# Kernel tuning notes

Hardware: AMD Instinct MI355X
Metric: run time of the kernel (lower is better)

The kernel has to match this reference:

```python
import jax, jax.numpy as jnp
import numpy as np

NB, H, C = 6, 4, 192
B, S, L = 2, 64, 256
VOCAB, ED = 24, 64


def setup_inputs() -> dict:
    key = jax.random.key(0)
    ks = iter(jax.random.split(key, 32))
    r = lambda sh: jax.random.normal(next(ks), sh, jnp.float32) * 0.02
    z = lambda sh: jnp.zeros(sh, jnp.float32)
    return {
        'tokens': jax.random.randint(next(ks), (B, S, L), 0, VOCAB, jnp.int32),
        'emb': r((VOCAB, ED)),
        'proj_w': r((C, ED)), 'proj_b': z((C,)),
        'ln_g': jnp.ones((NB, 3, C), jnp.float32), 'ln_b': z((NB, 3, C)),
        'wq': r((NB, 2, C, C)), 'wk': r((NB, 2, C, C)),
        'wv': r((NB, 2, C, C)), 'wo': r((NB, 2, C, C)),
        'bq': z((NB, 2, C)), 'bk': z((NB, 2, C)),
        'bv': z((NB, 2, C)), 'bo': z((NB, 2, C)),
        'ffn_w1': r((NB, 4 * C, C)), 'ffn_b1': z((NB, 4 * C)),
        'ffn_w2': r((NB, C, 4 * C)), 'ffn_b2': z((NB, C)),
        'pw_w': r((C,)), 'pw_b': z(()),
    }


def rotary(x):
    # ESM-style rotary embedding over positions along dim -2, feature dim last.
    d = x.shape[-1]
    inv = 1.0 / (10000.0 ** (jnp.arange(0, d, 2, dtype=jnp.float32) / d))
    t = jnp.arange(x.shape[-2], dtype=jnp.float32)
    f = t[:, None] * inv[None, :]                  # (pos, d/2)
    emb = jnp.concatenate([f, f], axis=-1)         # (pos, d)
    cos, sin = jnp.cos(emb), jnp.sin(emb)
    x1, x2 = jnp.split(x, 2, axis=-1)
    return x * cos + jnp.concatenate([-x2, x1], axis=-1) * sin


def ln_ch(x, g, b, eps=1e-5):
    # LayerNorm over channel axis 1 of (B,C,X,Y) (== transpose->LN->transpose).
    m = x.mean(axis=1, keepdims=True)
    v = jnp.var(x, axis=1, keepdims=True)
    return (x - m) * jax.lax.rsqrt(v + eps) * g[None, :, None, None] + b[None, :, None, None]


def lin_attn(x, wq, wk, wv, wo, bq, bk, bv, bo):
    # ScaledLinearAttention: elu+1 feature map, attends over dim -2 of (B,A,N,C).
    Bm, A, N, Cm = x.shape
    dh = Cm // H
    sh = lambda t: t.reshape(Bm, A, N, H, dh).transpose(0, 1, 3, 2, 4)  # (B,A,H,N,dh)
    q = sh(x @ wq.T + bq)
    k = sh(x @ wk.T + bk)
    v = sh(x @ wv.T + bv)
    q = (jax.nn.elu(q) + 1.0) / jnp.sqrt(jnp.float32(dh))
    k = jax.nn.elu(k) + 1.0
    kv = jnp.einsum('bahnd,bahne->bahde', k, v)
    z = 1.0 / (jnp.einsum('bahnd,bahd->bahn', q, k.sum(axis=-2)) + 1e-6)
    o = jnp.einsum('bahnd,bahde->bahne', q, kv) * z[..., None]
    o = o.transpose(0, 1, 3, 2, 4).reshape(Bm, A, N, Cm)
    return o @ wo.T + bo


def fwd(tokens, emb, proj_w, proj_b, ln_g, ln_b, wq, wk, wv, wo, bq, bk, bv, bo,
        ffn_w1, ffn_b1, ffn_w2, ffn_b2, pw_w, pw_b):
    x = emb[tokens]                    # (B,S,L,ED)
    x = x @ proj_w.T + proj_b          # (B,S,L,C)
    x = rotary(x)                      # rotary over L positions
    out = jnp.transpose(x, (0, 3, 1, 2))  # (B,C,S,L)
    for i in range(NB):
        # row attention (over L)
        h = ln_ch(out, ln_g[i, 0], ln_b[i, 0])
        h = jnp.transpose(h, (0, 2, 3, 1))  # (B,S,L,C)
        h = lin_attn(h, wq[i, 0], wk[i, 0], wv[i, 0], wo[i, 0],
                     bq[i, 0], bk[i, 0], bv[i, 0], bo[i, 0])
        out = out + jnp.transpose(h, (0, 3, 1, 2))
        # col attention (over S)
        h = ln_ch(out, ln_g[i, 1], ln_b[i, 1])
        h = jnp.transpose(h, (0, 3, 2, 1))  # (B,L,S,C)
        h = lin_attn(h, wq[i, 1], wk[i, 1], wv[i, 1], wo[i, 1],
                     bq[i, 1], bk[i, 1], bv[i, 1], bo[i, 1])
        out = out + jnp.transpose(h, (0, 3, 2, 1))
        # 1x1-conv FFN
        h = ln_ch(out, ln_g[i, 2], ln_b[i, 2])
        h = jnp.einsum('bcxy,oc->boxy', h, ffn_w1[i]) + ffn_b1[i][None, :, None, None]
        h = jax.nn.gelu(h, approximate=False)
        h = jnp.einsum('bcxy,oc->boxy', h, ffn_w2[i]) + ffn_b2[i][None, :, None, None]
        out = out + h
    o = jnp.einsum('bcxy,c->bxy', out, pw_w) + pw_b   # pwFNN 1x1 conv to 1 ch
    return jax.nn.sigmoid(jax.nn.softplus(o))


def reference(tokens, emb, proj_w, proj_b, ln_g, ln_b, wq, wk, wv, wo, bq, bk, bv, bo,
              ffn_w1, ffn_b1, ffn_w2, ffn_b2, pw_w, pw_b):
    return fwd(tokens, emb, proj_w, proj_b, ln_g, ln_b, wq, wk, wv, wo, bq, bk, bv, bo,
               ffn_w1, ffn_b1, ffn_w2, ffn_b2, pw_w, pw_b)
```

## Files before the change

### kernel.cpp

```cpp
#include <hip/hip_runtime.h>
#include <hip/hip_bf16.h>
#include <math.h>

#define NBLK 6
#define NH 4
#define CCH 192
#define BB 2
#define SS 64
#define LL 256
#define DH 48
#define NP (BB*SS*LL)
#define BUF ((size_t)NP*CCH)

typedef __attribute__((ext_vector_type(8))) short short8;
typedef __attribute__((ext_vector_type(4))) float float4v;

__device__ __forceinline__ unsigned short f2b(float f) {
    union { float f; unsigned int u; } v; v.f = f;
    unsigned int r = v.u + 0x7FFF + ((v.u >> 16) & 1);
    return (unsigned short)(r >> 16);
}
__device__ __forceinline__ float b2f(unsigned short u) {
    union { unsigned int u; float f; } v; v.u = ((unsigned int)u) << 16;
    return v.f;
}
__device__ __forceinline__ void async_lds16(const void* g, void* l) {
    __builtin_amdgcn_global_load_lds(
        (const __attribute__((address_space(1))) unsigned int*)g,
        (__attribute__((address_space(3))) unsigned int*)l, 16, 0, 0);
}

template<int N, int K>
__global__ void swz_conv(const float* __restrict__ src, unsigned short* __restrict__ dst, int layers) {
    int s = blockIdx.x * 256 + threadIdx.x;
    if (s >= layers * N * K) return;
    int li = s / (N * K);
    int t = s - li * (N * K);
    constexpr int KC = K / 32;
    int chunk = t >> 9, c = t & 511;
    int g = chunk / KC, sk = chunk - g * KC;
    int lane = c >> 3, ko = c & 7;
    int n = g * 16 + (lane & 15), k = sk * 32 + (lane >> 4) * 8 + ko;
    dst[s] = f2b(src[(size_t)li * N * K + (size_t)n * K + k]);
}
__global__ void wqkv_swz(const float* __restrict__ wq, const float* __restrict__ wk,
                         const float* __restrict__ wv, unsigned short* __restrict__ d) {
    int s = blockIdx.x * 256 + threadIdx.x;
    int wi = s / (576 * 192);
    int t = s - wi * 576 * 192;
    int chunk = t >> 9, c = t & 511;
    int g = chunk / 6, sk = chunk - g * 6;
    int lane = c >> 3, ko = c & 7;
    int n = g * 16 + (lane & 15), k = sk * 32 + (lane >> 4) * 8 + ko;
// ... 27 lines not shown
    int p = blockIdx.x * 4 + wave;
    int l = p & (LL - 1);
    const float* xp = Xt + (size_t)p * CCH;
    float v[3];
    #pragma unroll
    for (int i = 0; i < 3; ++i) {
        int c = lane + i * 64;
        int j = c % 96;
        float inv = expf((float)(2 * j) * (-9.210340371976184f / 192.0f));
        float ang = (float)l * inv;
        float part = (c < 96) ? -xp[c + 96] : xp[c - 96];
        v[i] = xp[c] * cosf(ang) + part * sinf(ang);
    }
    float s = v[0] + v[1] + v[2];
    float qq = v[0] * v[0] + v[1] * v[1] + v[2] * v[2];
    #pragma unroll
    for (int off = 32; off; off >>= 1) {
        s += __shfl_xor(s, off, 64);
        qq += __shfl_xor(qq, off, 64);
    }
    float mean = s * (1.0f / 192.0f);
    float var = qq * (1.0f / 192.0f) - mean * mean;
    float r = rsqrtf(var + 1e-5f);
    unsigned short* op = X + (size_t)p * CCH;
    unsigned short* hp = Hn + (size_t)p * CCH;
    #pragma unroll
    for (int i = 0; i < 3; ++i) {
        int c = lane + i * 64;
        op[c] = f2b(v[i]);
        hp[c] = f2b((v[i] - mean) * r * g[c] + b[c]);
    }
}

template<int MT, int EPI>
__global__ __launch_bounds__(256, (MT == 128) ? 3 : 4)
void mm192(const unsigned short* __restrict__ A, const unsigned short* __restrict__ Wsw,
           const float* __restrict__ bias,
           unsigned short* __restrict__ O0, unsigned short* __restrict__ O1,
           unsigned short* __restrict__ O2,
           float* __restrict__ Of,
           int M, int N, int K) {
    constexpr int NI = MT / 32;
    __shared__ __align__(16) unsigned char lds[(MT == 128) ? 51200 : 28672];
    const int tid = threadIdx.x;
    const int lane = tid & 63;
    const int w = tid >> 6;
    const int wm = w >> 1, wn = w & 1;
    const int m0 = blockIdx.y * MT;
    const int g0 = blockIdx.x * 12;
    const int q = lane >> 4;
    const int q8 = q << 3;
    const int r15 = lane & 15;
// ... 24 lines not shown
        #pragma unroll
        for (int i = 0; i < NI; ++i)
            #pragma unroll
            for (int j = 0; j < 6; ++j)
                acc[i][j] = __builtin_amdgcn_mfma_f32_16x16x32_bf16(af[i], wf[j], acc[i][j], 0, 0, 0);
    }

    const int nb = blockIdx.x * 192 + wn * 96 + r15;
    const int mb = m0 + wm * (MT / 2) + q * 4;

    if (EPI == 0) {
        unsigned short* TB = (unsigned short*)lds;
        const int bx = blockIdx.x;
        __syncthreads();
        #pragma unroll
        for (int j = 0; j < 6; ++j) {
            float bv = bias[nb + j * 16];
            #pragma unroll
            for (int i = 0; i < NI; ++i) {
                int row = wm * (MT / 2) + i * 16 + q * 4;
                #pragma unroll
                for (int r = 0; r < 4; ++r) {
                    float v = acc[i][j][r] + bv;
                    if (bx < 2) v = (v > 0.f) ? v + 1.f : expf(v);
                    if (bx == 0) v *= 0.14433756729740643f;
                    TB[(row + r) * 200 + wn * 96 + j * 16 + r15] = f2b(v);
                }
            }
        }
        __syncthreads();
        unsigned short* dst = (bx == 0) ? O0 : (bx == 1) ? O1 : O2;
        #pragma unroll
        for (int it = 0; it < (MT * 192) / 2048; ++it) {
            int idx = (it * 256 + tid) * 8;
            int row = idx / 192, col = idx - row * 192;
            *(short8*)(dst + (size_t)(m0 + row) * 192 + col) = *(const short8*)&TB[row * 200 + col];
        }
    } else {
        #pragma unroll
        for (int j = 0; j < 6; ++j) {
            int n = nb + j * 16;
            float bv = bias[n];
            #pragma unroll
            for (int i = 0; i < NI; ++i) {
                int mrow = mb + i * 16;
                #pragma unroll
                for (int r = 0; r < 4; ++r)
                    Of[(size_t)(mrow + r) * N + n] = acc[i][j][r] + bv;
            }
        }
    }
}


__global__ __launch_bounds__(512, 4)
void wo_qkv(const unsigned short* __restrict__ Ho,
            const unsigned short* __restrict__ WOs, const float* __restrict__ BO,
            unsigned short* __restrict__ Xres,
            const float* __restrict__ lng, const float* __restrict__ lnb,
            const unsigned short* __restrict__ QKVs, const float* __restrict__ bqkv,
            unsigned short* __restrict__ Qb, unsigned short* __restrict__ Kb,
            unsigned short* __restrict__ Vb) {
    __shared__ __align__(16) unsigned char lds[52224];
    unsigned char* Lo = lds;
    float* lsum = (float*)(lds + 25600);
    float* lsq  = lsum + 256;
    unsigned char* Ap = lds + 27648;
    const int tid = threadIdx.x;
    const int lane = tid & 63;
    const int w = tid >> 6;
    const int wm = w >> 2, wn = w & 3;
    const int m0 = blockIdx.x * 64;
    const int q = lane >> 4, q8 = q << 3, r15 = lane & 15;
    const int nb = wn * 48 + r15;

    #pragma unroll
    for (int it = 0; it < 3; ++it) {
        int c = it * 8 + w;
        int g = c / 6, sk = c - (c / 6) * 6;
        async_lds16(Ho + (size_t)(m0 + g * 16 + r15) * 192 + sk * 32 + q8, Lo + c * 1024);
    }
    __syncthreads();

    float4v acc[2][3];
    #pragma unroll
    for (int i = 0; i < 2; ++i)
        #pragma unroll
        for (int j = 0; j < 3; ++j)
            acc[i][j] = (float4v){0.f, 0.f, 0.f, 0.f};
    #pragma unroll
    for (int kk = 0; kk < 6; ++kk) {
        short8 af[2], wf[3];
        #pragma unroll
        for (int j = 0; j < 3; ++j)
            wf[j] = *(const short8*)(WOs + (((size_t)(wn * 3 + j) * 6 + kk) << 9) + lane * 8);
        #pragma unroll
        for (int i = 0; i < 2; ++i)
            af[i] = *(const short8*)(Lo + (((wm * 2 + i) * 6 + kk) << 10) + lane * 16);
        #pragma unroll
        for (int i = 0; i < 2; ++i)
            #pragma unroll
            for (int j = 0; j < 3; ++j)
                acc[i][j] = __builtin_amdgcn_mfma_f32_16x16x32_bf16(af[i], wf[j], acc[i][j], 0, 0, 0);
    }

    #pragma unroll
    for (int j = 0; j < 3; ++j) {
        int n = nb + j * 16;
        float bv = BO[n];
        #pragma unroll
        for (int i = 0; i < 2; ++i) {
            int mrow = m0 + wm * 32 + i * 16 + q * 4;
            #pragma unroll
            for (int r = 0; r < 4; ++r) {
                acc[i][j][r] += bv + b2f(Xres[(size_t)(mrow + r) * 192 + n]);
                Xres[(size_t)(mrow + r) * 192 + n] = f2b(acc[i][j][r]);
            }
        }
    }
    #pragma unroll
    for (int i = 0; i < 2; ++i)
        #pragma unroll
        for (int r = 0; r < 4; ++r) {
            float s1 = 0.f, s2 = 0.f;
            #pragma unroll
            for (int j = 0; j < 3; ++j) { float v = acc[i][j][r]; s1 += v; s2 += v * v; }
            #pragma unroll
            for (int off = 1; off < 16; off <<= 1) {
                s1 += __shfl_xor(s1, off, 64);
                s2 += __shfl_xor(s2, off, 64);
            }
            if (r15 == 0) {
                int rl = wm * 32 + i * 16 + q * 4 + r;
                lsum[rl * 4 + wn] = s1;
                lsq[rl * 4 + wn] = s2;
            }
        }
    __syncthreads();
    #pragma unroll
    for (int i = 0; i < 2; ++i) {
        int g = wm * 2 + i;
        #pragma unroll
        for (int r = 0; r < 4; ++r) {
            int rl = g * 16 + q * 4 + r;
            float mean = (lsum[rl * 4] + lsum[rl * 4 + 1] + lsum[rl * 4 + 2] + lsum[rl * 4 + 3]) * (1.0f / 192.0f);
            float var = (lsq[rl * 4] + lsq[rl * 4 + 1] + lsq[rl * 4 + 2] + lsq[rl * 4 + 3]) * (1.0f / 192.0f)
                      - mean * mean;
            float rstd = rsqrtf(var + 1e-5f);
            #pragma unroll
            for (int j = 0; j < 3; ++j) {
                int h = nb + j * 16;
                int base = (g * 6 + (h >> 5)) * 512 + ((h >> 3) & 3) * 128 + (h & 7);
                float v = (acc[i][j][r] - mean) * rstd * lng[h] + lnb[h];
                ((unsigned short*)Ap)[base + (q * 4 + r) * 8] = f2b(v);
            }
        }
    }
    __syncthreads();

    unsigned short* TB = (unsigned short*)Lo;
    for (int seg = 0; seg < 3; ++seg) {
        float4v a2[2][3];
        #pragma unroll
        for (int i = 0; i < 2; ++i)
            #pragma unroll
            for (int j = 0; j < 3; ++j)
                a2[i][j] = (float4v){0.f, 0.f, 0.f, 0.f};
        #pragma unroll
        for (int kk = 0; kk < 6; ++kk) {
            short8 af[2], wf[3];
            #pragma unroll
            for (int j = 0; j < 3; ++j)
                wf[j] = *(const short8*)(QKVs + (((size_t)(seg * 12 + wn * 3 + j) * 6 + kk) << 9) + lane * 8);
            #pragma unroll
            for (int i = 0; i < 2; ++i)
                af[i] = *(const short8*)(Ap + (((wm * 2 + i) * 6 + kk) << 10) + lane * 16);
            #pragma unroll
            for (int i = 0; i < 2; ++i)
                #pragma unroll
                for (int j = 0; j < 3; ++j)
                    a2[i][j] = __builtin_amdgcn_mfma_f32_16x16x32_bf16(af[i], wf[j], a2[i][j], 0, 0, 0);
        }
        __syncthreads();
        #pragma unroll
        for (int j = 0; j < 3; ++j) {
            float bv = bqkv[seg * 192 + nb + j * 16];
            #pragma unroll
            for (int i = 0; i < 2; ++i) {
                int row = wm * 32 + i * 16 + q * 4;
                #pragma unroll
                for (int r = 0; r < 4; ++r) {
                    float v = a2[i][j][r] + bv;
                    if (seg < 2) v = (v > 0.f) ? v + 1.f : expf(v);
                    if (seg == 0) v *= 0.14433756729740643f;
                    TB[(row + r) * 200 + nb + j * 16] = f2b(v);
                }
            }
        }
        __syncthreads();
        unsigned short* dst = (seg == 0) ? Qb : (seg == 1) ? Kb : Vb;
        #pragma unroll
        for (int it = 0; it < 3; ++it) {
            int idx = (it * 512 + tid) * 8;
            int row = idx / 192, col = idx - row * 192;
            *(short8*)(dst + (size_t)(m0 + row) * 192 + col) = *(const short8*)&TB[row * 200 + col];
        }
    }
}

template<bool LASTB>
__global__ __launch_bounds__(512, 4)
void wo_ffn_qkv(const unsigned short* __restrict__ Ho,
                const unsigned short* __restrict__ WOs, const float* __restrict__ BO,
                unsigned short* __restrict__ Xres,
                const float* __restrict__ ln1g, const float* __restrict__ ln1b,
                const unsigned short* __restrict__ W1s, const float* __restrict__ B1,
                const unsigned short* __restrict__ W2s, const float* __restrict__ B2,
                const float* __restrict__ ln2g, const float* __restrict__ ln2b,
                const unsigned short* __restrict__ QKVs, const float* __restrict__ bqkv,
                unsigned short* __restrict__ Qb, unsigned short* __restrict__ Kb,
                unsigned short* __restrict__ Vb) {
    __shared__ __align__(16) unsigned char lds[52224];
    unsigned char* Lo = lds;
    float* lsum = (float*)(lds + 25600);
    float* lsq  = lsum + 256;
    unsigned char* Ap = lds + 27648;
    const int tid = threadIdx.x;
    const int lane = tid & 63;
    const int w = tid >> 6;
    const int wm = w >> 2, wn = w & 3;
    const int m0 = blockIdx.x * 64;
    const int q = lane >> 4, q8 = q << 3, r15 = lane & 15;
    const int nb = wn * 48 + r15;

    #pragma unroll
    for (int it = 0; it < 3; ++it) {
        int c = it * 8 + w;
        int g = c / 6, sk = c - (c / 6) * 6;
        async_lds16(Ho + (size_t)(m0 + g * 16 + r15) * 192 + sk * 32 + q8, Lo + c * 1024);
    }
    __syncthreads();

    float4v xres[2][3];
    #pragma unroll
    for (int i = 0; i < 2; ++i)
        #pragma unroll
        for (int j = 0; j < 3; ++j)
            xres[i][j] = (float4v){0.f, 0.f, 0.f, 0.f};
    #pragma unroll
    for (int kk = 0; kk < 6; ++kk) {
        short8 af[2], wf[3];
        #pragma unroll
        for (int j = 0; j < 3; ++j)
            wf[j] = *(const short8*)(WOs + (((size_t)(wn * 3 + j) * 6 + kk) << 9) + lane * 8);
        #pragma unroll
        for (int i = 0; i < 2; ++i)
            af[i] = *(const short8*)(Lo + (((wm * 2 + i) * 6 + kk) << 10) + lane * 16);
        #pragma unroll
        for (int i = 0; i < 2; ++i)
            #pragma unroll
            for (int j = 0; j < 3; ++j)
                xres[i][j] = __builtin_amdgcn_mfma_f32_16x16x32_bf16(af[i], wf[j], xres[i][j], 0, 0, 0);
    }
    #pragma unroll
    for (int j = 0; j < 3; ++j) {
        int n = nb + j * 16;
        float bv = BO[n];
        #pragma unroll
        for (int i = 0; i < 2; ++i) {
            int mrow = m0 + wm * 32 + i * 16 + q * 4;
            #pragma unroll
            for (int r = 0; r < 4; ++r)
                xres[i][j][r] += bv + b2f(Xres[(size_t)(mrow + r) * 192 + n]);
        }
    }
    #pragma unroll
    for (int i = 0; i < 2; ++i)
        #pragma unroll
        for (int r = 0; r < 4; ++r) {
            float s1 = 0.f, s2 = 0.f;
            #pragma unroll
            for (int j = 0; j < 3; ++j) { float v = xres[i][j][r]; s1 += v; s2 += v * v; }
            #pragma unroll
            for (int off = 1; off < 16; off <<= 1) {
                s1 += __shfl_xor(s1, off, 64);
                s2 += __shfl_xor(s2, off, 64);
            }
            if (r15 == 0) {
                int rl = wm * 32 + i * 16 + q * 4 + r;
                lsum[rl * 4 + wn] = s1;
                lsq[rl * 4 + wn] = s2;
            }
        }
    __syncthreads();
    #pragma unroll
    for (int i = 0; i < 2; ++i) {
        int g = wm * 2 + i;
        #pragma unroll
        for (int r = 0; r < 4; ++r) {
            int rl = g * 16 + q * 4 + r;
            float mean = (lsum[rl * 4] + lsum[rl * 4 + 1] + lsum[rl * 4 + 2] + lsum[rl * 4 + 3]) * (1.0f / 192.0f);
            float var = (lsq[rl * 4] + lsq[rl * 4 + 1] + lsq[rl * 4 + 2] + lsq[rl * 4 + 3]) * (1.0f / 192.0f)
                      - mean * mean;
            float rstd = rsqrtf(var + 1e-5f);
            #pragma unroll
            for (int j = 0; j < 3; ++j) {
                int h = nb + j * 16;
                int base = (g * 6 + (h >> 5)) * 512 + ((h >> 3) & 3) * 128 + (h & 7);
                float v = (xres[i][j][r] - mean) * rstd * ln1g[h] + ln1b[h];
                ((unsigned short*)Ap)[base + (q * 4 + r) * 8] = f2b(v);
            }
        }
    }
    __syncthreads();

    float4v acc2[2][3];
    #pragma unroll
    for (int i = 0; i < 2; ++i)
        #pragma unroll
        for (int j = 0; j < 3; ++j)
            acc2[i][j] = (float4v){0.f, 0.f, 0.f, 0.f};
    for (int hc = 0; hc < 4; ++hc) {
        float4v acc1[2][3];
        #pragma unroll
        for (int i = 0; i < 2; ++i)
            #pragma unroll
            for (int j = 0; j < 3; ++j)
                acc1[i][j] = (float4v){0.f, 0.f, 0.f, 0.f};
        #pragma unroll
        for (int kk = 0; kk < 6; ++kk) {
            short8 af[2], wf[3];
            #pragma unroll
            for (int j = 0; j < 3; ++j)
                wf[j] = *(const short8*)(W1s + (((size_t)(hc * 12 + wn * 3 + j) * 6 + kk) << 9) + lane * 8);
            #pragma unroll
            for (int i = 0; i < 2; ++i)
                af[i] = *(const short8*)(Ap + (((wm * 2 + i) * 6 + kk) << 10) + lane * 16);
            #pragma unroll
            for (int i = 0; i < 2; ++i)
                #pragma unroll
                for (int j = 0; j < 3; ++j)
                    acc1[i][j] = __builtin_amdgcn_mfma_f32_16x16x32_bf16(af[i], wf[j], acc1[i][j], 0, 0, 0);
        }
        __syncthreads();
        #pragma unroll
        for (int i = 0; i < 2; ++i) {
            int g = wm * 2 + i;
            #pragma unroll
            for (int j = 0; j < 3; ++j) {
                int h = nb + j * 16;
                float bv = B1[hc * 192 + h];
                int base = (g * 6 + (h >> 5)) * 512 + ((h >> 3) & 3) * 128 + (h & 7);
                #pragma unroll
                for (int r = 0; r < 4; ++r) {
                    float v = acc1[i][j][r] + bv;
                    v = 0.5f * v * (1.0f + erff(v * 0.7071067811865475f));
                    ((unsigned short*)Lo)[base + (q * 4 + r) * 8] = f2b(v);
                }
            }
        }
        __syncthreads();
        #pragma unroll
        for (int kk = 0; kk < 6; ++kk) {
            short8 af[2], wf[3];
            #pragma unroll
            for (int j = 0; j < 3; ++j)
                wf[j] = *(const short8*)(W2s + (((size_t)(wn * 3 + j) * 24 + hc * 6 + kk) << 9) + lane * 8);
            #pragma unroll
            for (int i = 0; i < 2; ++i)
                af[i] = *(const short8*)(Lo + (((wm * 2 + i) * 6 + kk) << 10) + lane * 16);
            #pragma unroll
            for (int i = 0; i < 2; ++i)
                #pragma unroll
                for (int j = 0; j < 3; ++j)
                    acc2[i][j] = __builtin_amdgcn_mfma_f32_16x16x32_bf16(af[i], wf[j], acc2[i][j], 0, 0, 0);
        }
    }

    #pragma unroll
    for (int j = 0; j < 3; ++j) {
        int n = nb + j * 16;
        float bv = B2[n];
        #pragma unroll
        for (int i = 0; i < 2; ++i) {
            int mrow = m0 + wm * 32 + i * 16 + q * 4;
            #pragma unroll
            for (int r = 0; r < 4; ++r) {
                xres[i][j][r] += acc2[i][j][r] + bv;
                Xres[(size_t)(mrow + r) * 192 + n] = f2b(xres[i][j][r]);
            }
        }
    }
    if (LASTB) return;

    #pragma unroll
    for (int i = 0; i < 2; ++i)
        #pragma unroll
        for (int r = 0; r < 4; ++r) {
            float s1 = 0.f, s2 = 0.f;
            #pragma unroll
            for (int j = 0; j < 3; ++j) { float v = xres[i][j][r]; s1 += v; s2 += v * v; }
            #pragma unroll
            for (int off = 1; off < 16; off <<= 1) {
                s1 += __shfl_xor(s1, off, 64);
                s2 += __shfl_xor(s2, off, 64);
            }
            if (r15 == 0) {
                int rl = wm * 32 + i * 16 + q * 4 + r;
                lsum[rl * 4 + wn] = s1;
                lsq[rl * 4 + wn] = s2;
            }
        }
    __syncthreads();
    #pragma unroll
    for (int i = 0; i < 2; ++i) {
        int g = wm * 2 + i;
        #pragma unroll
        for (int r = 0; r < 4; ++r) {
            int rl = g * 16 + q * 4 + r;
            float mean = (lsum[rl * 4] + lsum[rl * 4 + 1] + lsum[rl * 4 + 2] + lsum[rl * 4 + 3]) * (1.0f / 192.0f);
            float var = (lsq[rl * 4] + lsq[rl * 4 + 1] + lsq[rl * 4 + 2] + lsq[rl * 4 + 3]) * (1.0f / 192.0f)
                      - mean * mean;
            float rstd = rsqrtf(var + 1e-5f);
            #pragma unroll
            for (int j = 0; j < 3; ++j) {
                int h = nb + j * 16;
                int base = (g * 6 + (h >> 5)) * 512 + ((h >> 3) & 3) * 128 + (h & 7);
                float v = (xres[i][j][r] - mean) * rstd * ln2g[h] + ln2b[h];
                ((unsigned short*)Ap)[base + (q * 4 + r) * 8] = f2b(v);
            }
        }
    }
    __syncthreads();

    unsigned short* TB = (unsigned short*)Lo;
    for (int seg = 0; seg < 3; ++seg) {
        float4v a2[2][3];
        #pragma unroll
        for (int i = 0; i < 2; ++i)
            #pragma unroll
            for (int j = 0; j < 3; ++j)
                a2[i][j] = (float4v){0.f, 0.f, 0.f, 0.f};
        #pragma unroll
        for (int kk = 0; kk < 6; ++kk) {
            short8 af[2], wf[3];
            #pragma unroll
            for (int j = 0; j < 3; ++j)
                wf[j] = *(const short8*)(QKVs + (((size_t)(seg * 12 + wn * 3 + j) * 6 + kk) << 9) + lane * 8);
            #pragma unroll
            for (int i = 0; i < 2; ++i)
                af[i] = *(const short8*)(Ap + (((wm * 2 + i) * 6 + kk) << 10) + lane * 16);
            #pragma unroll
            for (int i = 0; i < 2; ++i)
                #pragma unroll
                for (int j = 0; j < 3; ++j)
                    a2[i][j] = __builtin_amdgcn_mfma_f32_16x16x32_bf16(af[i], wf[j], a2[i][j], 0, 0, 0);
        }
        __syncthreads();
        #pragma unroll
        for (int j = 0; j < 3; ++j) {
            float bv = bqkv[seg * 192 + nb + j * 16];
            #pragma unroll
            for (int i = 0; i < 2; ++i) {
                int row = wm * 32 + i * 16 + q * 4;
                #pragma unroll
                for (int r = 0; r < 4; ++r) {
                    float v = a2[i][j][r] + bv;
                    if (seg < 2) v = (v > 0.f) ? v + 1.f : expf(v);
                    if (seg == 0) v *= 0.14433756729740643f;
                    TB[(row + r) * 200 + nb + j * 16] = f2b(v);
                }
            }
        }
        __syncthreads();
        unsigned short* dst = (seg == 0) ? Qb : (seg == 1) ? Kb : Vb;
        #pragma unroll
        for (int it = 0; it < 3; ++it) {
            int idx = (it * 512 + tid) * 8;
            int row = idx / 192, col = idx - row * 192;
            *(short8*)(dst + (size_t)(m0 + row) * 192 + col) = *(const short8*)&TB[row * 200 + col];
        }
    }
}

template<int N, int MSTR>
__global__ __launch_bounds__(256) void attn_axial(const unsigned short* __restrict__ Qb,
                                                  const unsigned short* __restrict__ Kb,
                                                  const unsigned short* __restrict__ Vb,
                                                  unsigned short* __restrict__ O) {
    __shared__ unsigned short KV[32][400];
    __shared__ unsigned short kvs[4][64][72];
    const int tid = threadIdx.x;
    const int lane = tid & 63;
    const int w = tid >> 6;
    const int q = lane >> 4, r15 = lane & 15, q8 = q * 8;
    size_t base;
    if (MSTR == 1) base = (size_t)blockIdx.x * N;
    else           base = (size_t)(blockIdx.x >> 8) * 16384 + (blockIdx.x & 255);

    unsigned int* kz = (unsigned int*)&kvs[w][0][0];
    #pragma unroll
// ... 71 lines not shown
            #pragma unroll
            for (int t = 0; t < 4; ++t)
                o[t] = __builtin_amdgcn_mfma_f32_16x16x32_bf16(aq, bkv[kk][t], o[t], 0, 0, 0);
        }
        #pragma unroll
        for (int r = 0; r < 4; ++r) {
            float den = __shfl(o[3][r], q << 4);
            float z = 1.0f / (den + 1e-6f);
            int n = mt * 16 + q * 4 + r;
            unsigned short* op = O + (base + (size_t)n * MSTR) * 192 + w * 48;
            #pragma unroll
            for (int t = 0; t < 3; ++t)
                op[t * 16 + r15] = f2b(o[t][r] * z);
        }
    }
}

__global__ __launch_bounds__(256) void final_kernel(const unsigned short* __restrict__ X,
                                                    const float* __restrict__ pw_w,
                                                    const float* __restrict__ pw_b, float* __restrict__ out) {
    int wave = threadIdx.x >> 6;
    int lane = threadIdx.x & 63;
    int p = blockIdx.x * 4 + wave;
    const unsigned short* xp = X + (size_t)p * CCH;
    float s = b2f(xp[lane]) * pw_w[lane] + b2f(xp[lane + 64]) * pw_w[lane + 64]
            + b2f(xp[lane + 128]) * pw_w[lane + 128];
    #pragma unroll
    for (int off = 32; off; off >>= 1) s += __shfl_xor(s, off, 64);
    if (lane == 0) {
        float o = s + pw_b[0];
        float e = expf(o);
        out[p] = 1.0f - 1.0f / (2.0f + e);
    }
}

extern "C" void kernel_launch(void* const* d_in, const int* in_sizes, int n_in,
                              void* d_out, int out_size, void* d_ws, size_t ws_size,
                              hipStream_t stream) {
    const int*   tokens = (const int*)  d_in[0];
    const float* emb    = (const float*)d_in[1];
    const float* proj_w = (const float*)d_in[2];
    const float* proj_b = (const float*)d_in[3];
    const float* ln_g   = (const float*)d_in[4];
    const float* ln_b   = (const float*)d_in[5];
    const float* wq     = (const float*)d_in[6];
    const float* wk     = (const float*)d_in[7];
    const float* wv     = (const float*)d_in[8];
    const float* wo     = (const float*)d_in[9];
    const float* bq     = (const float*)d_in[10];
// ... 21 lines not shown
    unsigned short* w1b = wob + WSZ;
    unsigned short* w2b = w1b + FSZ;
    unsigned short* pjb = w2b + FSZ;
    float* bqkvb = (float*)(pjb + 12288 + 32);
    float* Xt = (float*)Qb;

    wqkv_swz<<<QKVSZ / 256, 256, 0, stream>>>(wq, wk, wv, wqkvb);
    bqkv_concat<<<27, 256, 0, stream>>>(bq, bk, bv, bqkvb);
    swz_conv<192, 192><<<(WSZ + 255) / 256, 256, 0, stream>>>(wo, wob, NBLK * 2);
    swz_conv<768, 192><<<(FSZ + 255) / 256, 256, 0, stream>>>(ffn_w1, w1b, NBLK);
    swz_conv<192, 768><<<(FSZ + 255) / 256, 256, 0, stream>>>(ffn_w2, w2b, NBLK);
    swz_conv<192, 64><<<48, 256, 0, stream>>>(proj_w, pjb, 1);

    gather_kernel<<<NP * 64 / 256, 256, 0, stream>>>(tokens, emb, Eg);
    mm192<64, 1><<<dim3(1, NP / 64), 256, 0, stream>>>(Eg, pjb, proj_b,
                                                       nullptr, nullptr, nullptr, Xt, NP, CCH, 64);
    rotary_ln_kernel<<<NP / 4, 256, 0, stream>>>(Xt, X, Ho, ln_g, ln_b);
    mm192<128, 0><<<dim3(3, NP / 128), 256, 0, stream>>>(Ho, wqkvb, bqkvb,
                                                         Qb, Kb, Vb, nullptr, NP, 576, CCH);

    for (int i = 0; i < NBLK; ++i) {
        size_t wi0 = (size_t)(i * 2), wi1 = wi0 + 1;
        attn_axial<LL, 1><<<BB * SS, 256, 0, stream>>>(Qb, Kb, Vb, Ho);
        wo_qkv<<<NP / 64, 512, 0, stream>>>(Ho, wob + wi0 * CCH * CCH, bo + wi0 * CCH, X,
                                            ln_g + (size_t)(i * 3 + 1) * CCH, ln_b + (size_t)(i * 3 + 1) * CCH,
                                            wqkvb + wi1 * 576 * CCH, bqkvb + wi1 * 576, Qb, Kb, Vb);
        attn_axial<SS, LL><<<BB * LL, 256, 0, stream>>>(Qb, Kb, Vb, Ho);
        if (i < NBLK - 1) {
            size_t wn0 = (size_t)((i + 1) * 2);
            wo_ffn_qkv<false><<<NP / 64, 512, 0, stream>>>(
                Ho, wob + wi1 * CCH * CCH, bo + wi1 * CCH, X,
                ln_g + (size_t)(i * 3 + 2) * CCH, ln_b + (size_t)(i * 3 + 2) * CCH,
                w1b + (size_t)i * 768 * CCH, ffn_b1 + (size_t)i * 768,
                w2b + (size_t)i * CCH * 768, ffn_b2 + (size_t)i * CCH,
                ln_g + (size_t)((i + 1) * 3) * CCH, ln_b + (size_t)((i + 1) * 3) * CCH,
                wqkvb + wn0 * 576 * CCH, bqkvb + wn0 * 576, Qb, Kb, Vb);
        } else {
            wo_ffn_qkv<true><<<NP / 64, 512, 0, stream>>>(
                Ho, wob + wi1 * CCH * CCH, bo + wi1 * CCH, X,
                ln_g + (size_t)(i * 3 + 2) * CCH, ln_b + (size_t)(i * 3 + 2) * CCH,
                w1b + (size_t)i * 768 * CCH, ffn_b1 + (size_t)i * 768,
                w2b + (size_t)i * CCH * 768, ffn_b2 + (size_t)i * CCH,
                nullptr, nullptr, nullptr, nullptr, nullptr, nullptr, nullptr);
        }
    }
    final_kernel<<<NP / 4, 256, 0, stream>>>(X, pw_w, pw_b, (float*)d_out);
}
```

Measured before the change: 946.4 us.

## Shrink fused residual/FFN tiles to 32 rows and retile residual buffer

Changes the fused Wo/LN/QKV and Wo/FFN/QKV kernels from 512-thread, 64-row tiles to 256-thread, 32-row tiles with half the LDS, doubling the grid. The residual stream X is stored in a 16-row interleaved layout so each lane reads and writes four consecutive rows as one 8-byte access, and bf16 stores use the packed v_cvt_pk_bf16 instruction. It also switches expf to __expf and adds a fast erf-polynomial GELU. The cost is more blocks, each re-reading the weights, plus some loss of exp and GELU accuracy.

```diff
diff --git a/kernel.cpp b/kernel.cpp
--- a/kernel.cpp
+++ b/kernel.cpp
@@ -14,6 +14,7 @@
 
 typedef __attribute__((ext_vector_type(8))) short short8;
 typedef __attribute__((ext_vector_type(4))) float float4v;
+typedef __attribute__((ext_vector_type(2))) unsigned int uintx2;
 
 __device__ __forceinline__ unsigned short f2b(float f) {
     union { float f; unsigned int u; } v; v.f = f;
@@ -24,11 +25,44 @@
     union { unsigned int u; float f; } v; v.u = ((unsigned int)u) << 16;
     return v.f;
 }
+__device__ __forceinline__ unsigned int cvt_pk_bf16(float lo, float hi) {
+    unsigned int r;
+    asm("v_cvt_pk_bf16_f32 %0, %1, %2" : "=v"(r) : "v"(lo), "v"(hi));
+    return r;
+}
+__device__ __forceinline__ void st2u(unsigned short* p0, unsigned short* p1, float a, float b) {
+    unsigned int u = cvt_pk_bf16(a, b);
+    *p0 = (unsigned short)u;
+    *p1 = (unsigned short)(u >> 16);
+}
+__device__ __forceinline__ void xf_unpack(uintx2 u, float* f) {
+    union { unsigned int x; float ff; } t;
+    t.x = u[0] << 16;          f[0] = t.ff;
+    t.x = u[0] & 0xffff0000u;  f[1] = t.ff;
+    t.x = u[1] << 16;          f[2] = t.ff;
+    t.x = u[1] & 0xffff0000u;  f[3] = t.ff;
+}
+__device__ __forceinline__ float gelu_f(float v) {
+    float z = v * 0.7071067811865475f;
+    float a = fabsf(z);
+    float t = __builtin_amdgcn_rcpf(fmaf(0.3275911f, a, 1.0f));
+    float p = fmaf(t, 1.061405429f, -1.453152027f);
+    p = fmaf(t, p, 1.421413741f);
+    p = fmaf(t, p, -0.284496736f);
+    p = fmaf(t, p, 0.254829592f);
+    p *= t;
+    float e = __expf(-a * a);
+    float er = fmaf(-p, e, 1.0f);
+    er = __builtin_copysignf(er, z);
+    return 0.5f * v * (1.0f + er);
+}
 __device__ __forceinline__ void async_lds16(const void* g, void* l) {
     __builtin_amdgcn_global_load_lds(
         (const __attribute__((address_space(1))) unsigned int*)g,
         (__attribute__((address_space(3))) unsigned int*)l, 16, 0, 0);
 }
+
+#define XF(p16, c) (((size_t)(p16) * 192 + (c)) << 4)
 
 template<int N, int K>
 __global__ void swz_conv(const float* __restrict__ src, unsigned short* __restrict__ dst, int layers) {
@@ -102,12 +136,12 @@
     float mean = s * (1.0f / 192.0f);
     float var = qq * (1.0f / 192.0f) - mean * mean;
     float r = rsqrtf(var + 1e-5f);
-    unsigned short* op = X + (size_t)p * CCH;
     unsigned short* hp = Hn + (size_t)p * CCH;
+    const int p16 = p >> 4, pr = p & 15;
     #pragma unroll
     for (int i = 0; i < 3; ++i) {
         int c = lane + i * 64;
-        op[c] = f2b(v[i]);
+        X[XF(p16, c) + pr] = f2b(v[i]);
         hp[c] = f2b((v[i] - mean) * r * g[c] + b[c]);
     }
 }
@@ -178,7 +212,7 @@
                 #pragma unroll
                 for (int r = 0; r < 4; ++r) {
                     float v = acc[i][j][r] + bv;
-                    if (bx < 2) v = (v > 0.f) ? v + 1.f : expf(v);
+                    if (bx < 2) v = (v > 0.f) ? v + 1.f : __expf(v);
                     if (bx == 0) v *= 0.14433756729740643f;
                     TB[(row + r) * 200 + wn * 96 + j * 16 + r15] = f2b(v);
                 }
@@ -209,7 +243,7 @@
 }
 
 
-__global__ __launch_bounds__(512, 4)
+__global__ __launch_bounds__(256, 4)
 void wo_qkv(const unsigned short* __restrict__ Ho,
             const unsigned short* __restrict__ WOs, const float* __restrict__ BO,
             unsigned short* __restrict__ Xres,
@@ -217,23 +251,22 @@
             const unsigned short* __restrict__ QKVs, const float* __restrict__ bqkv,
             unsigned short* __restrict__ Qb, unsigned short* __restrict__ Kb,
             unsigned short* __restrict__ Vb) {
-    __shared__ __align__(16) unsigned char lds[52224];
+    __shared__ __align__(16) unsigned char lds[26112];
     unsigned char* Lo = lds;
-    float* lsum = (float*)(lds + 25600);
-    float* lsq  = lsum + 256;
-    unsigned char* Ap = lds + 27648;
+    float* lsum = (float*)(lds + 12800);
+    float* lsq  = lsum + 128;
+    unsigned char* Ap = lds + 13824;
     const int tid = threadIdx.x;
     const int lane = tid & 63;
     const int w = tid >> 6;
-    const int wm = w >> 2, wn = w & 3;
-    const int m0 = blockIdx.x * 64;
+    const int m0 = blockIdx.x * 32;
     const int q = lane >> 4, q8 = q << 3, r15 = lane & 15;
-    const int nb = wn * 48 + r15;
+    const int nb = w * 48 + r15;
 
     #pragma unroll
     for (int it = 0; it < 3; ++it) {
-        int c = it * 8 + w;
-        int g = c / 6, sk = c - (c / 6) * 6;
+        int c = it * 4 + w;
+        int g = c / 6, sk = c - g * 6;
         async_lds16(Ho + (size_t)(m0 + g * 16 + r15) * 192 + sk * 32 + q8, Lo + c * 1024);
     }
     __syncthreads();
@@ -249,10 +282,10 @@
         short8 af[2], wf[3];
         #pragma unroll
         for (int j = 0; j < 3; ++j)
-            wf[j] = *(const short8*)(WOs + (((size_t)(wn * 3 + j) * 6 + kk) << 9) + lane * 8);
+            wf[j] = *(const short8*)(WOs + (((size_t)(w * 3 + j) * 6 + kk) << 9) + lane * 8);
         #pragma unroll
         for (int i = 0; i < 2; ++i)
-            af[i] = *(const short8*)(Lo + (((wm * 2 + i) * 6 + kk) << 10) + lane * 16);
+            af[i] = *(const short8*)(Lo + ((i * 6 + kk) << 10) + lane * 16);
         #pragma unroll
         for (int i = 0; i < 2; ++i)
             #pragma unroll
@@ -266,50 +299,59 @@
         float bv = BO[n];
         #pragma unroll
         for (int i = 0; i < 2; ++i) {
-            int mrow = m0 + wm * 32 + i * 16 + q * 4;
-            #pragma unroll
-            for (int r = 0; r < 4; ++r) {
-                acc[i][j][r] += bv + b2f(Xres[(size_t)(mrow + r) * 192 + n]);
-                Xres[(size_t)(mrow + r) * 192 + n] = f2b(acc[i][j][r]);
-            }
+            unsigned short* xp = Xres + XF(blockIdx.x * 2 + i, n) + q * 4;
+            uintx2 u = *(const uintx2*)xp;
+            float f[4]; xf_unpack(u, f);
+            #pragma unroll
+            for (int r = 0; r < 4; ++r) acc[i][j][r] += bv + f[r];
+            uintx2 o;
+            o[0] = cvt_pk_bf16(acc[i][j][0], acc[i][j][1]);
+            o[1] = cvt_pk_bf16(acc[i][j][2], acc[i][j][3]);
+            *(uintx2*)xp = o;
         }
     }
     #pragma unroll
     for (int i = 0; i < 2; ++i)
         #pragma unroll
         for (int r = 0; r < 4; ++r) {
-            float s1 = 0.f, s2 = 0.f;
-            #pragma unroll
-            for (int j = 0; j < 3; ++j) { float v = acc[i][j][r]; s1 += v; s2 += v * v; }
+            float s1 = acc[i][0][r] + acc[i][1][r] + acc[i][2][r];
+            float s2 = acc[i][0][r] * acc[i][0][r] + acc[i][1][r] * acc[i][1][r] + acc[i][2][r] * acc[i][2][r];
             #pragma unroll
             for (int off = 1; off < 16; off <<= 1) {
                 s1 += __shfl_xor(s1, off, 64);
                 s2 += __shfl_xor(s2, off, 64);
             }
             if (r15 == 0) {
-                int rl = wm * 32 + i * 16 + q * 4 + r;
-                lsum[rl * 4 + wn] = s1;
-                lsq[rl * 4 + wn] = s2;
+                int rl = i * 16 + q * 4 + r;
+                lsum[rl * 4 + w] = s1;
+                lsq[rl * 4 + w] = s2;
             }
         }
     __syncthreads();
     #pragma unroll
     for (int i = 0; i < 2; ++i) {
-        int g = wm * 2 + i;
+        float mean[4], rstd[4];
         #pragma unroll
         for (int r = 0; r < 4; ++r) {
-            int rl = g * 16 + q * 4 + r;
-            float mean = (lsum[rl * 4] + lsum[rl * 4 + 1] + lsum[rl * 4 + 2] + lsum[rl * 4 + 3]) * (1.0f / 192.0f);
-            float var = (lsq[rl * 4] + lsq[rl * 4 + 1] + lsq[rl * 4 + 2] + lsq[rl * 4 + 3]) * (1.0f / 192.0f)
-                      - mean * mean;
-            float rstd = rsqrtf(var + 1e-5f);
-            #pragma unroll
-            for (int j = 0; j < 3; ++j) {
-                int h = nb + j * 16;
-                int base = (g * 6 + (h >> 5)) * 512 + ((h >> 3) & 3) * 128 + (h & 7);
-                float v = (acc[i][j][r] - mean) * rstd * lng[h] + lnb[h];
-                ((unsigned short*)Ap)[base + (q * 4 + r) * 8] = f2b(v);
-            }
+            int rl4 = (i * 16 + q * 4 + r) * 4;
+            float s  = lsum[rl4] + lsum[rl4 + 1] + lsum[rl4 + 2] + lsum[rl4 + 3];
+            float ss = lsq[rl4] + lsq[rl4 + 1] + lsq[rl4 + 2] + lsq[rl4 + 3];
+            float m = s * (1.0f / 192.0f);
+            mean[r] = m;
+            rstd[r] = rsqrtf(ss * (1.0f / 192.0f) - m * m + 1e-5f);
+        }
+        #pragma unroll
+        for (int j = 0; j < 3; ++j) {
+            int h = nb + j * 16;
+            float gg = lng[h], bb = lnb[h];
+            unsigned short* ap = (unsigned short*)Ap + (i * 6 + (h >> 5)) * 512
+                               + ((h >> 3) & 3) * 128 + (h & 7) + q * 32;
+            float v0 = (acc[i][j][0] - mean[0]) * rstd[0] * gg + bb;
+            float v1 = (acc[i][j][1] - mean[1]) * rstd[1] * gg + bb;
+            float v2 = (acc[i][j][2] - mean[2]) * rstd[2] * gg + bb;
+            float v3 = (acc[i][j][3] - mean[3]) * rstd[3] * gg + bb;
+            st2u(ap, ap + 8, v0, v1);
+            st2u(ap + 16, ap + 24, v2, v3);
         }
     }
     __syncthreads();
@@ -327,10 +369,10 @@
             short8 af[2], wf[3];
             #pragma unroll
             for (int j = 0; j < 3; ++j)
-                wf[j] = *(const short8*)(QKVs + (((size_t)(seg * 12 + wn * 3 + j) * 6 + kk) << 9) + lane * 8);
+                wf[j] = *(const short8*)(QKVs + (((size_t)(seg * 12 + w * 3 + j) * 6 + kk) << 9) + lane * 8);
             #pragma unroll
             for (int i = 0; i < 2; ++i)
-                af[i] = *(const short8*)(Ap + (((wm * 2 + i) * 6 + kk) << 10) + lane * 16);
+                af[i] = *(const short8*)(Ap + ((i * 6 + kk) << 10) + lane * 16);
             #pragma unroll
             for (int i = 0; i < 2; ++i)
                 #pragma unroll
@@ -343,21 +385,25 @@
             float bv = bqkv[seg * 192 + nb + j * 16];
             #pragma unroll
             for (int i = 0; i < 2; ++i) {
-                int row = wm * 32 + i * 16 + q * 4;
+                int row = i * 16 + q * 4;
+                float v[4];
                 #pragma unroll
                 for (int r = 0; r < 4; ++r) {
-                    float v = a2[i][j][r] + bv;
-                    if (seg < 2) v = (v > 0.f) ? v + 1.f : expf(v);
-                    if (seg == 0) v *= 0.14433756729740643f;
-                    TB[(row + r) * 200 + nb + j * 16] = f2b(v);
+                    float x = a2[i][j][r] + bv;
+                    if (seg < 2) x = (x > 0.f) ? x + 1.f : __expf(x);
+                    if (seg == 0) x *= 0.14433756729740643f;
+                    v[r] = x;
                 }
+                unsigned short* tp = &TB[row * 200 + nb + j * 16];
+                st2u(tp, tp + 200, v[0], v[1]);
+                st2u(tp + 400, tp + 600, v[2], v[3]);
             }
         }
         __syncthreads();
         unsigned short* dst = (seg == 0) ? Qb : (seg == 1) ? Kb : Vb;
         #pragma unroll
         for (int it = 0; it < 3; ++it) {
-            int idx = (it * 512 + tid) * 8;
+            int idx = (it * 256 + tid) * 8;
             int row = idx / 192, col = idx - row * 192;
             *(short8*)(dst + (size_t)(m0 + row) * 192 + col) = *(const short8*)&TB[row * 200 + col];
         }
@@ -365,7 +411,7 @@
 }
 
 template<bool LASTB>
-__global__ __launch_bounds__(512, 4)
+__global__ __launch_bounds__(256, 4)
 void wo_ffn_qkv(const unsigned short* __restrict__ Ho,
                 const unsigned short* __restrict__ WOs, const float* __restrict__ BO,
                 unsigned short* __restrict__ Xres,
@@ -376,23 +422,22 @@
                 const unsigned short* __restrict__ QKVs, const float* __restrict__ bqkv,
                 unsigned short* __restrict__ Qb, unsigned short* __restrict__ Kb,
                 unsigned short* __restrict__ Vb) {
-    __shared__ __align__(16) unsigned char lds[52224];
+    __shared__ __align__(16) unsigned char lds[26112];
     unsigned char* Lo = lds;
-    float* lsum = (float*)(lds + 25600);
-    float* lsq  = lsum + 256;
-    unsigned char* Ap = lds + 27648;
+    float* lsum = (float*)(lds + 12800);
+    float* lsq  = lsum + 128;
+    unsigned char* Ap = lds + 13824;
     const int tid = threadIdx.x;
     const int lane = tid & 63;
     const int w = tid >> 6;
-    const int wm = w >> 2, wn = w & 3;
-    const int m0 = blockIdx.x * 64;
+    const int m0 = blockIdx.x * 32;
     const int q = lane >> 4, q8 = q << 3, r15 = lane & 15;
-    const int nb = wn * 48 + r15;
+    const int nb = w * 48 + r15;
 
     #pragma unroll
     for (int it = 0; it < 3; ++it) {
-        int c = it * 8 + w;
-        int g = c / 6, sk = c - (c / 6) * 6;
+        int c = it * 4 + w;
+        int g = c / 6, sk = c - g * 6;
         async_lds16(Ho + (size_t)(m0 + g * 16 + r15) * 192 + sk * 32 + q8, Lo + c * 1024);
     }
     __syncthreads();
@@ -408,10 +453,10 @@
         short8 af[2], wf[3];
         #pragma unroll
         for (int j = 0; j < 3; ++j)
-            wf[j] = *(const short8*)(WOs + (((size_t)(wn * 3 + j) * 6 + kk) << 9) + lane * 8);
+            wf[j] = *(const short8*)(WOs + (((size_t)(w * 3 + j) * 6 + kk) << 9) + lane * 8);
         #pragma unroll
         for (int i = 0; i < 2; ++i)
-            af[i] = *(const short8*)(Lo + (((wm * 2 + i) * 6 + kk) << 10) + lane * 16);
+            af[i] = *(const short8*)(Lo + ((i * 6 + kk) << 10) + lane * 16);
         #pragma unroll
         for (int i = 0; i < 2; ++i)
             #pragma unroll
@@ -424,48 +469,55 @@
         float bv = BO[n];
         #pragma unroll
         for (int i = 0; i < 2; ++i) {
-            int mrow = m0 + wm * 32 + i * 16 + q * 4;
-            #pragma unroll
-            for (int r = 0; r < 4; ++r)
-                xres[i][j][r] += bv + b2f(Xres[(size_t)(mrow + r) * 192 + n]);
+            const unsigned short* xp = Xres + XF(blockIdx.x * 2 + i, n) + q * 4;
+            uintx2 u = *(const uintx2*)xp;
+            float f[4]; xf_unpack(u, f);
+            #pragma unroll
+            for (int r = 0; r < 4; ++r) xres[i][j][r] += bv + f[r];
         }
     }
     #pragma unroll
     for (int i = 0; i < 2; ++i)
         #pragma unroll
         for (int r = 0; r < 4; ++r) {
-            float s1 = 0.f, s2 = 0.f;
-            #pragma unroll
-            for (int j = 0; j < 3; ++j) { float v = xres[i][j][r]; s1 += v; s2 += v * v; }
+            float s1 = xres[i][0][r] + xres[i][1][r] + xres[i][2][r];
+            float s2 = xres[i][0][r] * xres[i][0][r] + xres[i][1][r] * xres[i][1][r] + xres[i][2][r] * xres[i][2][r];
             #pragma unroll
             for (int off = 1; off < 16; off <<= 1) {
                 s1 += __shfl_xor(s1, off, 64);
                 s2 += __shfl_xor(s2, off, 64);
             }
             if (r15 == 0) {
-                int rl = wm * 32 + i * 16 + q * 4 + r;
-                lsum[rl * 4 + wn] = s1;
-                lsq[rl * 4 + wn] = s2;
+                int rl = i * 16 + q * 4 + r;
+                lsum[rl * 4 + w] = s1;
+                lsq[rl * 4 + w] = s2;
             }
         }
     __syncthreads();
     #pragma unroll
     for (int i = 0; i < 2; ++i) {
-        int g = wm * 2 + i;
+        float mean[4], rstd[4];
         #pragma unroll
         for (int r = 0; r < 4; ++r) {
-            int rl = g * 16 + q * 4 + r;
-            float mean = (lsum[rl * 4] + lsum[rl * 4 + 1] + lsum[rl * 4 + 2] + lsum[rl * 4 + 3]) * (1.0f / 192.0f);
-            float var = (lsq[rl * 4] + lsq[rl * 4 + 1] + lsq[rl * 4 + 2] + lsq[rl * 4 + 3]) * (1.0f / 192.0f)
-                      - mean * mean;
-            float rstd = rsqrtf(var + 1e-5f);
-            #pragma unroll
-            for (int j = 0; j < 3; ++j) {
-                int h = nb + j * 16;
-                int base = (g * 6 + (h >> 5)) * 512 + ((h >> 3) & 3) * 128 + (h & 7);
-                float v = (xres[i][j][r] - mean) * rstd * ln1g[h] + ln1b[h];
-                ((unsigned short*)Ap)[base + (q * 4 + r) * 8] = f2b(v);
-            }
+            int rl4 = (i * 16 + q * 4 + r) * 4;
+            float s  = lsum[rl4] + lsum[rl4 + 1] + lsum[rl4 + 2] + lsum[rl4 + 3];
+            float ss = lsq[rl4] + lsq[rl4 + 1] + lsq[rl4 + 2] + lsq[rl4 + 3];
+            float m = s * (1.0f / 192.0f);
+            mean[r] = m;
+            rstd[r] = rsqrtf(ss * (1.0f / 192.0f) - m * m + 1e-5f);
+        }
+        #pragma unroll
+        for (int j = 0; j < 3; ++j) {
+            int h = nb + j * 16;
+            float gg = ln1g[h], bb = ln1b[h];
+            unsigned short* ap = (unsigned short*)Ap + (i * 6 + (h >> 5)) * 512
+                               + ((h >> 3) & 3) * 128 + (h & 7) + q * 32;
+            float v0 = (xres[i][j][0] - mean[0]) * rstd[0] * gg + bb;
+            float v1 = (xres[i][j][1] - mean[1]) * rstd[1] * gg + bb;
+            float v2 = (xres[i][j][2] - mean[2]) * rstd[2] * gg + bb;
+            float v3 = (xres[i][j][3] - mean[3]) * rstd[3] * gg + bb;
+            st2u(ap, ap + 8, v0, v1);
+            st2u(ap + 16, ap + 24, v2, v3);
         }
     }
     __syncthreads();
@@ -488,10 +540,10 @@
             short8 af[2], wf[3];
             #pragma unroll
             for (int j = 0; j < 3; ++j)
-                wf[j] = *(const short8*)(W1s + (((size_t)(hc * 12 + wn * 3 + j) * 6 + kk) << 9) + lane * 8);
+                wf[j] = *(const short8*)(W1s + (((size_t)(hc * 12 + w * 3 + j) * 6 + kk) << 9) + lane * 8);
             #pragma unroll
             for (int i = 0; i < 2; ++i)
-                af[i] = *(const short8*)(Ap + (((wm * 2 + i) * 6 + kk) << 10) + lane * 16);
+                af[i] = *(const short8*)(Ap + ((i * 6 + kk) << 10) + lane * 16);
             #pragma unroll
             for (int i = 0; i < 2; ++i)
                 #pragma unroll
@@ -500,31 +552,30 @@
         }
         __syncthreads();
         #pragma unroll
-        for (int i = 0; i < 2; ++i) {
-            int g = wm * 2 + i;
+        for (int i = 0; i < 2; ++i)
             #pragma unroll
             for (int j = 0; j < 3; ++j) {
                 int h = nb + j * 16;
                 float bv = B1[hc * 192 + h];
-                int base = (g * 6 + (h >> 5)) * 512 + ((h >> 3) & 3) * 128 + (h & 7);
-                #pragma unroll
-                for (int r = 0; r < 4; ++r) {
-                    float v = acc1[i][j][r] + bv;
-                    v = 0.5f * v * (1.0f + erff(v * 0.7071067811865475f));
-                    ((unsigned short*)Lo)[base + (q * 4 + r) * 8] = f2b(v);
-                }
-            }
-        }
+                unsigned short* lp = (unsigned short*)Lo + (i * 6 + (h >> 5)) * 512
+                                   + ((h >> 3) & 3) * 128 + (h & 7) + q * 32;
+                float v0 = gelu_f(acc1[i][j][0] + bv);
+                float v1 = gelu_f(acc1[i][j][1] + bv);
+                float v2 = gelu_f(acc1[i][j][2] + bv);
+                float v3 = gelu_f(acc1[i][j][3] + bv);
+                st2u(lp, lp + 8, v0, v1);
+                st2u(lp + 16, lp + 24, v2, v3);
+            }
         __syncthreads();
         #pragma unroll
         for (int kk = 0; kk < 6; ++kk) {
             short8 af[2], wf[3];
             #pragma unroll
             for (int j = 0; j < 3; ++j)
-                wf[j] = *(const short8*)(W2s + (((size_t)(wn * 3 + j) * 24 + hc * 6 + kk) << 9) + lane * 8);
+                wf[j] = *(const short8*)(W2s + (((size_t)(w * 3 + j) * 24 + hc * 6 + kk) << 9) + lane * 8);
             #pragma unroll
             for (int i = 0; i < 2; ++i)
-                af[i] = *(const short8*)(Lo + (((wm * 2 + i) * 6 + kk) << 10) + lane * 16);
+                af[i] = *(const short8*)(Lo + ((i * 6 + kk) << 10) + lane * 16);
             #pragma unroll
             for (int i = 0; i < 2; ++i)
                 #pragma unroll
@@ -539,12 +590,14 @@
         float bv = B2[n];
         #pragma unroll
         for (int i = 0; i < 2; ++i) {
-            int mrow = m0 + wm * 32 + i * 16 + q * 4;
-            #pragma unroll
-            for (int r = 0; r < 4; ++r) {
+            #pragma unroll
+            for (int r = 0; r < 4; ++r)
                 xres[i][j][r] += acc2[i][j][r] + bv;
-                Xres[(size_t)(mrow + r) * 192 + n] = f2b(xres[i][j][r]);
-            }
+            unsigned short* xp = Xres + XF(blockIdx.x * 2 + i, n) + q * 4;
+            uintx2 o;
+            o[0] = cvt_pk_bf16(xres[i][j][0], xres[i][j][1]);
+            o[1] = cvt_pk_bf16(xres[i][j][2], xres[i][j][3]);
+            *(uintx2*)xp = o;
         }
     }
     if (LASTB) return;
@@ -553,38 +606,44 @@
     for (int i = 0; i < 2; ++i)
         #pragma unroll
         for (int r = 0; r < 4; ++r) {
-            float s1 = 0.f, s2 = 0.f;
-            #pragma unroll
-            for (int j = 0; j < 3; ++j) { float v = xres[i][j][r]; s1 += v; s2 += v * v; }
+            float s1 = xres[i][0][r] + xres[i][1][r] + xres[i][2][r];
+            float s2 = xres[i][0][r] * xres[i][0][r] + xres[i][1][r] * xres[i][1][r] + xres[i][2][r] * xres[i][2][r];
             #pragma unroll
             for (int off = 1; off < 16; off <<= 1) {
                 s1 += __shfl_xor(s1, off, 64);
                 s2 += __shfl_xor(s2, off, 64);
             }
             if (r15 == 0) {
-                int rl = wm * 32 + i * 16 + q * 4 + r;
-                lsum[rl * 4 + wn] = s1;
-                lsq[rl * 4 + wn] = s2;
+                int rl = i * 16 + q * 4 + r;
+                lsum[rl * 4 + w] = s1;
+                lsq[rl * 4 + w] = s2;
             }
         }
     __syncthreads();
     #pragma unroll
     for (int i = 0; i < 2; ++i) {
-        int g = wm * 2 + i;
+        float mean[4], rstd[4];
         #pragma unroll
         for (int r = 0; r < 4; ++r) {
-            int rl = g * 16 + q * 4 + r;
-            float mean = (lsum[rl * 4] + lsum[rl * 4 + 1] + lsum[rl * 4 + 2] + lsum[rl * 4 + 3]) * (1.0f / 192.0f);
-            float var = (lsq[rl * 4] + lsq[rl * 4 + 1] + lsq[rl * 4 + 2] + lsq[rl * 4 + 3]) * (1.0f / 192.0f)
-                      - mean * mean;
-            float rstd = rsqrtf(var + 1e-5f);
-            #pragma unroll
-            for (int j = 0; j < 3; ++j) {
-                int h = nb + j * 16;
-                int base = (g * 6 + (h >> 5)) * 512 + ((h >> 3) & 3) * 128 + (h & 7);
-                float v = (xres[i][j][r] - mean) * rstd * ln2g[h] + ln2b[h];
-                ((unsigned short*)Ap)[base + (q * 4 + r) * 8] = f2b(v);
-            }
+            int rl4 = (i * 16 + q * 4 + r) * 4;
+            float s  = lsum[rl4] + lsum[rl4 + 1] + lsum[rl4 + 2] + lsum[rl4 + 3];
+            float ss = lsq[rl4] + lsq[rl4 + 1] + lsq[rl4 + 2] + lsq[rl4 + 3];
+            float m = s * (1.0f / 192.0f);
+            mean[r] = m;
+            rstd[r] = rsqrtf(ss * (1.0f / 192.0f) - m * m + 1e-5f);
+        }
+        #pragma unroll
+        for (int j = 0; j < 3; ++j) {
+            int h = nb + j * 16;
+            float gg = ln2g[h], bb = ln2b[h];
+            unsigned short* ap = (unsigned short*)Ap + (i * 6 + (h >> 5)) * 512
+                               + ((h >> 3) & 3) * 128 + (h & 7) + q * 32;
+            float v0 = (xres[i][j][0] - mean[0]) * rstd[0] * gg + bb;
+            float v1 = (xres[i][j][1] - mean[1]) * rstd[1] * gg + bb;
+            float v2 = (xres[i][j][2] - mean[2]) * rstd[2] * gg + bb;
+            float v3 = (xres[i][j][3] - mean[3]) * rstd[3] * gg + bb;
+            st2u(ap, ap + 8, v0, v1);
+            st2u(ap + 16, ap + 24, v2, v3);
         }
     }
     __syncthreads();
@@ -602,10 +661,10 @@
             short8 af[2], wf[3];
             #pragma unroll
             for (int j = 0; j < 3; ++j)
-                wf[j] = *(const short8*)(QKVs + (((size_t)(seg * 12 + wn * 3 + j) * 6 + kk) << 9) + lane * 8);
+                wf[j] = *(const short8*)(QKVs + (((size_t)(seg * 12 + w * 3 + j) * 6 + kk) << 9) + lane * 8);
             #pragma unroll
             for (int i = 0; i < 2; ++i)
-                af[i] = *(const short8*)(Ap + (((wm * 2 + i) * 6 + kk) << 10) + lane * 16);
+                af[i] = *(const short8*)(Ap + ((i * 6 + kk) << 10) + lane * 16);
             #pragma unroll
             for (int i = 0; i < 2; ++i)
                 #pragma unroll
@@ -618,21 +677,25 @@
             float bv = bqkv[seg * 192 + nb + j * 16];
             #pragma unroll
             for (int i = 0; i < 2; ++i) {
-                int row = wm * 32 + i * 16 + q * 4;
+                int row = i * 16 + q * 4;
+                float v[4];
                 #pragma unroll
                 for (int r = 0; r < 4; ++r) {
-                    float v = a2[i][j][r] + bv;
-                    if (seg < 2) v = (v > 0.f) ? v + 1.f : expf(v);
-                    if (seg == 0) v *= 0.14433756729740643f;
-                    TB[(row + r) * 200 + nb + j * 16] = f2b(v);
+                    float x = a2[i][j][r] + bv;
+                    if (seg < 2) x = (x > 0.f) ? x + 1.f : __expf(x);
+                    if (seg == 0) x *= 0.14433756729740643f;
+                    v[r] = x;
                 }
+                unsigned short* tp = &TB[row * 200 + nb + j * 16];
+                st2u(tp, tp + 200, v[0], v[1]);
+                st2u(tp + 400, tp + 600, v[2], v[3]);
             }
         }
         __syncthreads();
         unsigned short* dst = (seg == 0) ? Qb : (seg == 1) ? Kb : Vb;
         #pragma unroll
         for (int it = 0; it < 3; ++it) {
-            int idx = (it * 512 + tid) * 8;
+            int idx = (it * 256 + tid) * 8;
             int row = idx / 192, col = idx - row * 192;
             *(short8*)(dst + (size_t)(m0 + row) * 192 + col) = *(const short8*)&TB[row * 200 + col];
         }
@@ -750,9 +813,10 @@
     int wave = threadIdx.x >> 6;
     int lane = threadIdx.x & 63;
     int p = blockIdx.x * 4 + wave;
-    const unsigned short* xp = X + (size_t)p * CCH;
-    float s = b2f(xp[lane]) * pw_w[lane] + b2f(xp[lane + 64]) * pw_w[lane + 64]
-            + b2f(xp[lane + 128]) * pw_w[lane + 128];
+    const unsigned short* xp = X + XF(p >> 4, 0) + (p & 15);
+    float s = b2f(xp[(size_t)lane << 4]) * pw_w[lane]
+            + b2f(xp[(size_t)(lane + 64) << 4]) * pw_w[lane + 64]
+            + b2f(xp[(size_t)(lane + 128) << 4]) * pw_w[lane + 128];
     #pragma unroll
     for (int off = 32; off; off >>= 1) s += __shfl_xor(s, off, 64);
     if (lane == 0) {
@@ -820,13 +884,13 @@
     for (int i = 0; i < NBLK; ++i) {
         size_t wi0 = (size_t)(i * 2), wi1 = wi0 + 1;
         attn_axial<LL, 1><<<BB * SS, 256, 0, stream>>>(Qb, Kb, Vb, Ho);
-        wo_qkv<<<NP / 64, 512, 0, stream>>>(Ho, wob + wi0 * CCH * CCH, bo + wi0 * CCH, X,
+        wo_qkv<<<NP / 32, 256, 0, stream>>>(Ho, wob + wi0 * CCH * CCH, bo + wi0 * CCH, X,
                                             ln_g + (size_t)(i * 3 + 1) * CCH, ln_b + (size_t)(i * 3 + 1) * CCH,
                                             wqkvb + wi1 * 576 * CCH, bqkvb + wi1 * 576, Qb, Kb, Vb);
         attn_axial<SS, LL><<<BB * LL, 256, 0, stream>>>(Qb, Kb, Vb, Ho);
         if (i < NBLK - 1) {
             size_t wn0 = (size_t)((i + 1) * 2);
-            wo_ffn_qkv<false><<<NP / 64, 512, 0, stream>>>(
+            wo_ffn_qkv<false><<<NP / 32, 256, 0, stream>>>(
                 Ho, wob + wi1 * CCH * CCH, bo + wi1 * CCH, X,
                 ln_g + (size_t)(i * 3 + 2) * CCH, ln_b + (size_t)(i * 3 + 2) * CCH,
                 w1b + (size_t)i * 768 * CCH, ffn_b1 + (size_t)i * 768,
@@ -834,7 +898,7 @@
                 ln_g + (size_t)((i + 1) * 3) * CCH, ln_b + (size_t)((i + 1) * 3) * CCH,
                 wqkvb + wn0 * 576 * CCH, bqkvb + wn0 * 576, Qb, Kb, Vb);
         } else {
-            wo_ffn_qkv<true><<<NP / 64, 512, 0, stream>>>(
+            wo_ffn_qkv<true><<<NP / 32, 256, 0, stream>>>(
                 Ho, wob + wi1 * CCH * CCH, bo + wi1 * CCH, X,
                 ln_g + (size_t)(i * 3 + 2) * CCH, ln_b + (size_t)(i * 3 + 2) * CCH,
                 w1b + (size_t)i * 768 * CCH, ffn_b1 + (size_t)i * 768,
```

Result: faster. 918.0 us (-3.0%).
